# Performance work log

Measured on AMD Instinct MI355X. Metric: run time of the kernel, lower is better.

Reference implementation:

```python
import jax, jax.numpy as jnp
import numpy as np
import math

D_MODEL = 1024
N_HEADS = 16
RANK = 16
SCALE = 16.0
T_LEN = 2048
BSZ = 2


def setup_inputs() -> dict:
    key = jax.random.key(0)
    ks = jax.random.split(key, 12)
    d, r = D_MODEL, RANK
    inp = {
        "query": jax.random.normal(ks[0], (T_LEN, BSZ, d), dtype=jnp.float32),
        "key": jax.random.normal(ks[1], (T_LEN, BSZ, d), dtype=jnp.float32),
        "value": jax.random.normal(ks[2], (T_LEN, BSZ, d), dtype=jnp.float32),
        "need_weights": 0,
        "attn_mask": 0,
        "in_proj_weight": jax.random.normal(ks[3], (3 * d, d), dtype=jnp.float32) * 0.02,
        "in_proj_bias": jax.random.normal(ks[4], (3 * d,), dtype=jnp.float32) * 0.02,
        "out_w": jax.random.normal(ks[5], (d, d), dtype=jnp.float32) * 0.02,
        "out_b": jax.random.normal(ks[6], (d,), dtype=jnp.float32) * 0.02,
        "k_a": jax.random.normal(ks[7], (r, d), dtype=jnp.float32) * 0.02,
        "k_b": jax.random.normal(ks[8], (r, d), dtype=jnp.float32) * 0.02,
        "v_a": jax.random.normal(ks[9], (r, d), dtype=jnp.float32) * 0.02,
        "v_b": jax.random.normal(ks[10], (r, d), dtype=jnp.float32) * 0.02,
    }
    return inp


def reference(query, key, value, need_weights, attn_mask,
              in_proj_weight, in_proj_bias, out_w, out_b,
              k_a, k_b, v_a, v_b):
    # NOTE: original module computes q,k,v all from `query` (self-attention);
    # `key`, `value`, `need_weights`, `attn_mask` are unused in the math.
    T, B, d = query.shape
    H = N_HEADS
    hd = d // H
    qkv = query @ in_proj_weight.T + in_proj_bias  # (T, B, 3d)
    q, k, v = jnp.split(qkv, 3, axis=-1)
    s = SCALE / RANK
    # LoRA low-rank updates on K and V (computed from query)
    k = k + s * ((query @ k_a.T) @ k_b)
    v = v + s * ((query @ v_a.T) @ v_b)
    # split heads: (T, B, H, hd)
    qh = q.reshape(T, B, H, hd)
    kh = k.reshape(T, B, H, hd)
    vh = v.reshape(T, B, H, hd)
    scale = 1.0 / math.sqrt(hd)
    scores = jnp.einsum('tbhd,sbhd->bhts', qh * scale, kh)  # (B, H, T, T)
    attn = jax.nn.softmax(scores, axis=-1)
    out = jnp.einsum('bhts,sbhd->tbhd', attn, vh).reshape(T, B, d)
    out = out @ out_w.T + out_b
    return out
```

## Files before the change

kernel.cpp:

```cpp
#include <hip/hip_runtime.h>
#include <stdint.h>

#define DEVI __device__ __forceinline__

typedef unsigned short u16;
typedef __attribute__((ext_vector_type(4))) float f32x4;
typedef __attribute__((ext_vector_type(16))) float f32x16;
typedef __attribute__((ext_vector_type(8))) short bf16x8;
typedef __attribute__((ext_vector_type(2))) unsigned int u32x2;

constexpr int T_LEN = 2048;
constexpr int BSZ   = 2;
constexpr int DM    = 1024;
constexpr int NH    = 16;
constexpr int HD    = 64;
constexpr int MROWS = T_LEN * BSZ;
constexpr float LORA_S = 16.0f / 16.0f;
constexpr float QSCALE = 0.125f * 1.4426950408889634f;

DEVI u16 f2bf(float x) {
  union { float f; uint32_t u; } v; v.f = x;
  uint32_t r = (v.u + 0x7FFFu + ((v.u >> 16) & 1u)) >> 16;
  return (u16)r;
}

DEVI uint32_t pk2bf(float a, float b) {
  return (uint32_t)f2bf(a) | ((uint32_t)f2bf(b) << 16);
}

DEVI uint32_t e2r(float x) {
  union { float f; uint32_t u; } v;
  v.f = __builtin_amdgcn_exp2f(x);
  return v.u;
}

DEVI void gload_lds16(const void* g, void* l) {
  __builtin_amdgcn_global_load_lds(
      (const __attribute__((address_space(1))) void*)g,
      (__attribute__((address_space(3))) void*)l, 16, 0, 0);
}

DEVI f32x4 mfma16(bf16x8 a, bf16x8 b, f32x4 c) {
  return __builtin_amdgcn_mfma_f32_16x16x32_bf16(a, b, c, 0, 0, 0);
}
DEVI f32x16 mfma32(bf16x8 a, bf16x8 b, f32x16 c) {
  return __builtin_amdgcn_mfma_f32_32x32x16_bf16(a, b, c, 0, 0, 0);
}

DEVI int kvswz(int rc, int l) { return rc * 128 + ((l ^ (rc & 15)) << 3); }

#define WAITBAR(N)                                        \
  do {                                                    \
    asm volatile("s_waitcnt vmcnt(" #N ")" ::: "memory"); \
    __builtin_amdgcn_sched_barrier(0);                    \
    __builtin_amdgcn_s_barrier();                         \
    __builtin_amdgcn_sched_barrier(0);                    \
  } while (0)

#define BARO()                                            \
  do {                                                    \
    __builtin_amdgcn_sched_barrier(0);                    \
    __builtin_amdgcn_s_barrier();                         \
    __builtin_amdgcn_sched_barrier(0);                    \
  } while (0)

__global__ void prep_kernel(const float* __restrict__ query,
                            const float* __restrict__ W,
                            const float* __restrict__ ka, const float* __restrict__ kb,
                            const float* __restrict__ va, const float* __restrict__ vb,
                            const float* __restrict__ ow,
                            u16* __restrict__ Wm, u16* __restrict__ Wo,
                            u16* __restrict__ Aq) {
  const int W3 = 3 * DM * DM;
  const int WO = DM * DM;
  const int AQ = MROWS * DM;
  const int total = W3 + WO + AQ;
  for (int idx = blockIdx.x * blockDim.x + threadIdx.x; idx < total;
       idx += gridDim.x * blockDim.x) {
    if (idx < W3) {
      const int n = idx >> 10, k = idx & 1023;
      float w = W[idx];
      if (n >= 2 * DM) {
        const int n2 = n - 2 * DM;
        float a = 0.f;
#pragma unroll
        for (int r = 0; r < 16; ++r) a += va[r * DM + k] * vb[r * DM + n2];
        w += LORA_S * a;
      } else if (n >= DM) {
        const int n2 = n - DM;
        float a = 0.f;
#pragma unroll
        for (int r = 0; r < 16; ++r) a += ka[r * DM + k] * kb[r * DM + n2];
        w += LORA_S * a;
      }
      Wm[idx] = f2bf(w);
    } else if (idx < W3 + WO) {
      const int i = idx - W3;
      Wo[i] = f2bf(ow[i]);
    } else {
      const int i = idx - W3 - WO;
      Aq[i] = f2bf(query[i]);
    }
  }
}

template <int EPIL>
__global__ __launch_bounds__(256) void gemm_bt(
    const u16* __restrict__ A, const u16* __restrict__ Bt,
    const float* __restrict__ bias, float* __restrict__ Cf,
    u16* __restrict__ Qb, u16* __restrict__ Kb, u16* __restrict__ Vt,
    int M, int N, int K) {
  constexpr int BM = 128, BN = 128, BK = 32;
  __shared__ alignas(16) u16 SM[4][2][4096];
  const int tid = threadIdx.x;
  const int wv = tid >> 6, ln = tid & 63;
  const int l16 = ln & 15, lhi = ln >> 4;
  const int row0 = blockIdx.x * BM, col0 = blockIdx.y * BN;
  const int wr = (wv >> 1) * 64, wc = (wv & 1) * 64;

  f32x4 acc[4][4];
#pragma unroll
  for (int i = 0; i < 4; ++i)
#pragma unroll
    for (int j2 = 0; j2 < 4; ++j2) acc[i][j2] = f32x4{0.f, 0.f, 0.f, 0.f};

  const int lrA = wv * 16 + (ln >> 3);
  const int lrB = lrA + 8;
  const int s_ = ln & 7;
  const int la = s_ ^ (lrA & 7), lb = s_ ^ (lrB & 7);
  const int ra = lrA + 64 * (la >> 2), ca = (la & 3) * 8;
  const int rb = lrB + 64 * (lb >> 2), cb = (lb & 3) * 8;

  const u16* pa0 = A + (size_t)(row0 + ra) * K + ca;
  const u16* pa1 = A + (size_t)(row0 + rb) * K + cb;
  const u16* pb0 = Bt + (size_t)(col0 + ra) * K + ca;
  const u16* pb1 = Bt + (size_t)(col0 + rb) * K + cb;

  auto stagep = [&](int buf) {
    gload_lds16(pa0, &SM[buf][0][(wv * 16) * 64]);
    gload_lds16(pa1, &SM[buf][0][(wv * 16 + 8) * 64]);
    gload_lds16(pb0, &SM[buf][1][(wv * 16) * 64]);
    gload_lds16(pb1, &SM[buf][1][(wv * 16 + 8) * 64]);
    pa0 += BK; pa1 += BK; pb0 += BK; pb1 += BK;
  };

  auto compute = [&](int buf) {
    const u16* Al = SM[buf][0];
    const u16* Bl = SM[buf][1];
    bf16x8 af[4], bfr[4];
#pragma unroll
    for (int m = 0; m < 4; ++m) {
      const int r = wr + m * 16 + l16, lr = r & 63;
      const int sl = (lhi | ((r >> 6) << 2)) ^ (lr & 7);
      af[m] = *(const bf16x8*)&Al[lr * 64 + sl * 8];
    }
#pragma unroll
    for (int n = 0; n < 4; ++n) {
      const int r = wc + n * 16 + l16, lr = r & 63;
      const int sl = (lhi | ((r >> 6) << 2)) ^ (lr & 7);
      bfr[n] = *(const bf16x8*)&Bl[lr * 64 + sl * 8];
    }
#pragma unroll
    for (int m = 0; m < 4; ++m)
#pragma unroll
      for (int n = 0; n < 4; ++n) acc[m][n] = mfma16(af[m], bfr[n], acc[m][n]);
  };

  const int NS = K / BK;
  stagep(0); stagep(1); stagep(2);

  for (int t4 = 0; t4 < NS - 4; t4 += 4) {
    WAITBAR(8); compute(0); stagep(3);
    WAITBAR(8); compute(1); stagep(0);
    WAITBAR(8); compute(2); stagep(1);
    WAITBAR(8); compute(3); stagep(2);
  }
  WAITBAR(8); compute(0); stagep(3);
  WAITBAR(8); compute(1);
  WAITBAR(4); compute(2);
  WAITBAR(0); compute(3);

  if constexpr (EPIL == 0) {
    if (col0 >= 2 * DM) {
      u16* Cl = (u16*)SM;
      __syncthreads();
#pragma unroll
      for (int m = 0; m < 4; ++m)
#pragma unroll
        for (int n = 0; n < 4; ++n) {
          const int lc = wc + n * 16 + l16;
          const float bc = bias[col0 + lc];
#pragma unroll
          for (int r = 0; r < 4; ++r) {
            const int rl = wr + m * 16 + lhi * 4 + r;
            const int tl = rl >> 1, bb = rl & 1;
            Cl[lc * 128 + bb * 64 + (((tl >> 3) ^ (lc & 7)) << 3) + (tl & 7)] =
                f2bf(acc[m][n][r] + bc);
          }
        }
      __syncthreads();
      const int h0 = (col0 - 2 * DM) >> 6;
      const int t0 = row0 >> 1;
#pragma unroll
      for (int i = 0; i < 8; ++i) {
        const int cid = i * 256 + tid;
        const int lc = cid >> 4, bb = (cid >> 3) & 1, tc = cid & 7;
        bf16x8 ch = *(const bf16x8*)&Cl[lc * 128 + bb * 64 + ((tc ^ (lc & 7)) << 3)];
        const int h = h0 + (lc >> 6), dd = lc & 63;
        *(bf16x8*)&Vt[(((size_t)(bb * NH + h)) * HD + dd) * T_LEN + t0 + tc * 8] = ch;
      }
      return;
    }
  }

#pragma unroll
  for (int m = 0; m < 4; ++m) {
#pragma unroll
    for (int n = 0; n < 4; ++n) {
      const int col = col0 + wc + n * 16 + l16;
      const float bc = bias[col];
#pragma unroll
      for (int r = 0; r < 4; ++r) {
        const int row = row0 + wr + m * 16 + lhi * 4 + r;
        const float v = acc[m][n][r] + bc;
        if constexpr (EPIL == 0) {
          const int t = row >> 1, b = row & 1;
          if (col < DM) {
            const int h = col >> 6, dd = col & 63;
            Qb[(((size_t)(b * NH + h)) * T_LEN + t) * HD + dd] = f2bf(v * QSCALE);
          } else {
            const int c2 = col - DM, h = c2 >> 6, dd = c2 & 63;
            Kb[(((size_t)(b * NH + h)) * T_LEN + t) * HD + dd] = f2bf(v);
          }
        } else {
          Cf[(size_t)row * N + col] = v;
        }
      }
    }
  }
}

__global__ __launch_bounds__(256) void attn_kernel(const u16* __restrict__ Qb,
                                                   const u16* __restrict__ Kb,
                                                   const u16* __restrict__ Vt,
                                                   u16* __restrict__ Ob) {
  constexpr int KBLK = 64;
  __shared__ alignas(16) u16 KV[4][2][32 * 128];

  const int tid = threadIdx.x;
  const int wv = tid >> 6, ln = tid & 63;
  const int l32 = ln & 31, hi = ln >> 5;

  const int bid = blockIdx.x;
  const int lb = (bid & 7) * 64 + (bid >> 3);
  const int bh = lb >> 4;
  const int b = bh >> 4, h = bh & 15;
  const int q0 = (lb & 15) * 128 + wv * 32;

  const u16* Qh = Qb + (size_t)bh * T_LEN * HD;
  const u16* Kh = Kb + (size_t)bh * T_LEN * HD;
  const u16* Vh = Vt + (size_t)bh * HD * T_LEN;

  bf16x8 qf[4];
#pragma unroll
  for (int kd = 0; kd < 4; ++kd)
    qf[kd] = *(const bf16x8*)&Qh[(size_t)(q0 + l32) * HD + kd * 16 + hi * 8];

  bf16x8 ones;
#pragma unroll
  for (int i = 0; i < 8; ++i) ones[i] = (short)0x3F80;

  f32x16 ot[2] = {f32x16{}, f32x16{}};
  f32x16 lacc = f32x16{};

  const int g_row = ln >> 4;
  const int g_s   = ln & 15;
  const int j0 = wv * 2, j1 = wv * 2 + 1;
  const int row0r = 4 * j0 + g_row, row1r = 4 * j1 + g_row;
  const int l0 = g_s ^ (row0r & 15), l1 = g_s ^ (row1r & 15);
  const int lr0 = row0r + 32 * (l0 >> 3), lr1 = row1r + 32 * (l1 >> 3);
  const int c80 = (l0 & 7) * 8, c81 = (l1 & 7) * 8;

  const u16* ks0 = Kh + (size_t)lr0 * HD + c80;
  const u16* ks1 = Kh + (size_t)lr1 * HD + c81;
  const u16* vs0 = Vh + (size_t)lr0 * T_LEN + c80;
  const u16* vs1 = Vh + (size_t)lr1 * T_LEN + c81;

  auto stagep = [&](int buf) {
    gload_lds16(ks0, &KV[buf][0][j0 * 512]);
    gload_lds16(ks1, &KV[buf][0][j1 * 512]);
    gload_lds16(vs0, &KV[buf][1][j0 * 512]);
    gload_lds16(vs1, &KV[buf][1][j1 * 512]);
    ks0 += KBLK * HD; ks1 += KBLK * HD; vs0 += KBLK; vs1 += KBLK;
  };

  auto compute = [&](int buf) {
    const u16* Kl = KV[buf][0];
    const u16* Vl = KV[buf][1];
    f32x16 st[2] = {f32x16{}, f32x16{}};
    __builtin_amdgcn_s_setprio(1);
#pragma unroll
    for (int kd = 0; kd < 4; ++kd) {
      bf16x8 k0 = *(const bf16x8*)&Kl[kvswz(l32, kd * 2 + hi)];
      bf16x8 k1 = *(const bf16x8*)&Kl[kvswz(l32, 8 + kd * 2 + hi)];
      st[0] = mfma32(k0, qf[kd], st[0]);
      st[1] = mfma32(k1, qf[kd], st[1]);
    }
    __builtin_amdgcn_s_setprio(0);
    uint32_t c[2][8];
#pragma unroll
    for (int mk = 0; mk < 2; ++mk)
#pragma unroll
      for (int d = 0; d < 8; ++d)
        c[mk][d] = __builtin_amdgcn_perm(e2r(st[mk][2 * d + 1]),
                                         e2r(st[mk][2 * d]), 0x07060302u);
    __builtin_amdgcn_s_setprio(1);
#pragma unroll
    for (int ksl = 0; ksl < 4; ++ksl) {
      const int mk = ksl >> 1, s2 = ksl & 1;
      uint32_t a0 = c[mk][4 * s2 + 0], b0 = c[mk][4 * s2 + 2];
      uint32_t a1 = c[mk][4 * s2 + 1], b1 = c[mk][4 * s2 + 3];
      u32x2 r0 = __builtin_amdgcn_permlane32_swap(a0, b0, false, false);
      u32x2 r1 = __builtin_amdgcn_permlane32_swap(a1, b1, false, false);
      union { bf16x8 v; uint32_t u[4]; } pu;
      pu.u[0] = r0[0]; pu.u[1] = r1[0]; pu.u[2] = r0[1]; pu.u[3] = r1[1];
      bf16x8 vf0 = *(const bf16x8*)&Vl[kvswz(l32, ksl * 2 + hi)];
      bf16x8 vf1 = *(const bf16x8*)&Vl[kvswz(l32, 8 + ksl * 2 + hi)];
      ot[0] = mfma32(vf0, pu.v, ot[0]);
      ot[1] = mfma32(vf1, pu.v, ot[1]);
      lacc = mfma32(ones, pu.v, lacc);
    }
    __builtin_amdgcn_s_setprio(0);
  };

  stagep(0); stagep(1); stagep(2); stagep(3);

  for (int it7 = 0; it7 < 7; ++it7) {
    WAITBAR(8); compute(0); compute(1); BARO(); stagep(0); stagep(1);
    WAITBAR(8); compute(2); compute(3); BARO(); stagep(2); stagep(3);
  }
  WAITBAR(8); compute(0); compute(1);
  WAITBAR(0); compute(2); compute(3);

  const float inv = 1.0f / lacc[0];
  const size_t rowbase = ((size_t)(q0 + l32) * BSZ + b) * DM + h * HD;
#pragma unroll
  for (int dt = 0; dt < 2; ++dt) {
#pragma unroll
    for (int g = 0; g < 4; ++g) {
      const float v0 = ot[dt][4 * g + 0] * inv;
      const float v1 = ot[dt][4 * g + 1] * inv;
      const float v2 = ot[dt][4 * g + 2] * inv;
      const float v3 = ot[dt][4 * g + 3] * inv;
      u32x2 w; w[0] = pk2bf(v0, v1); w[1] = pk2bf(v2, v3);
      const int dim = dt * 32 + 8 * g + 4 * hi;
      *(u32x2*)&Ob[rowbase + dim] = w;
    }
  }
}

extern "C" void kernel_launch(void* const* d_in, const int* in_sizes, int n_in,
                              void* d_out, int out_size, void* d_ws, size_t ws_size,
                              hipStream_t stream) {
  const float* query = (const float*)d_in[0];
  const float* W     = (const float*)d_in[5];
  const float* bias  = (const float*)d_in[6];
  const float* ow    = (const float*)d_in[7];
  const float* ob    = (const float*)d_in[8];
  const float* ka    = (const float*)d_in[9];
  const float* kb    = (const float*)d_in[10];
  const float* va    = (const float*)d_in[11];
  const float* vb    = (const float*)d_in[12];

  char* ws = (char*)d_ws;
  u16* Wm = (u16*)ws; ws += (size_t)3 * DM * DM * 2;
  u16* Wo = (u16*)ws; ws += (size_t)DM * DM * 2;
  u16* Aq = (u16*)ws; ws += (size_t)MROWS * DM * 2;
  u16* Qb = (u16*)ws; ws += (size_t)BSZ * NH * T_LEN * HD * 2;
  u16* Kb = (u16*)ws; ws += (size_t)BSZ * NH * T_LEN * HD * 2;
  u16* Vt = (u16*)ws; ws += (size_t)BSZ * NH * T_LEN * HD * 2;
  u16* Ob = (u16*)ws; ws += (size_t)MROWS * DM * 2;

  prep_kernel<<<2048, 256, 0, stream>>>(query, W, ka, kb, va, vb, ow, Wm, Wo, Aq);

  gemm_bt<0><<<dim3(MROWS / 128, (3 * DM) / 128), 256, 0, stream>>>(
      Aq, Wm, bias, nullptr, Qb, Kb, Vt, MROWS, 3 * DM, DM);

  attn_kernel<<<512, 256, 0, stream>>>(Qb, Kb, Vt, Ob);

  gemm_bt<1><<<dim3(MROWS / 128, DM / 128), 256, 0, stream>>>(
      Ob, Wo, ob, (float*)d_out, nullptr, nullptr, nullptr, MROWS, DM, DM);
}
```

Baseline: 109.7 us.

## Use 256x256-tile, 512-thread GEMM for the fused QKV projection

Adds a dedicated QKV projection kernel with 256x256 output tiles and 8 waves per block in place of the 128x128 templated GEMM, and strips the QKV epilogue from the generic GEMM. Larger tiles double operand reuse from LDS and halve global loads per FLOP, and s_setprio raises the MFMA wave priority. In exchange the grid drops to 16x12=192 blocks, which may underfill the GPU's compute units, and the bigger accumulator footprint raises register pressure.

```diff
diff --git a/kernel.cpp b/kernel.cpp
--- a/kernel.cpp
+++ b/kernel.cpp
@@ -104,6 +104,135 @@
   }
 }
 
+__global__ __launch_bounds__(512) void gemm256_qkv(
+    const u16* __restrict__ A, const u16* __restrict__ Bt,
+    const float* __restrict__ bias,
+    u16* __restrict__ Qb, u16* __restrict__ Kb, u16* __restrict__ Vt) {
+  constexpr int K = DM;
+  constexpr int BK = 32;
+  __shared__ alignas(16) u16 SM[4][2][128 * 64];
+  const int tid = threadIdx.x;
+  const int wv = tid >> 6, ln = tid & 63;
+  const int l16 = ln & 15, lhi = ln >> 4;
+  const int wm = wv >> 2, wn = wv & 3;
+  const int row0 = blockIdx.x * 256, col0 = blockIdx.y * 256;
+
+  f32x4 acc[8][4];
+#pragma unroll
+  for (int m = 0; m < 8; ++m)
+#pragma unroll
+    for (int n = 0; n < 4; ++n) acc[m][n] = f32x4{0.f, 0.f, 0.f, 0.f};
+
+  const int rr0 = wv * 16 + (ln >> 3);
+  const int sl_ = ln & 7;
+  const int v0 = sl_ ^ (rr0 & 7);
+  const int lrow0 = rr0 + 128 * (v0 >> 2);
+  const int c0 = (v0 & 3) * 8;
+
+  const u16* pa = A + (size_t)(row0 + lrow0) * K + c0;
+  const u16* pb = Bt + (size_t)(col0 + lrow0) * K + c0;
+
+  auto stagep = [&](int buf) {
+    gload_lds16(pa, &SM[buf][0][(wv * 16) * 64]);
+    gload_lds16(pa + (size_t)8 * K, &SM[buf][0][(wv * 16 + 8) * 64]);
+    gload_lds16(pb, &SM[buf][1][(wv * 16) * 64]);
+    gload_lds16(pb + (size_t)8 * K, &SM[buf][1][(wv * 16 + 8) * 64]);
+    pa += BK; pb += BK;
+  };
+
+  auto compute = [&](int buf) {
+    const u16* Al = SM[buf][0];
+    const u16* Bl = SM[buf][1];
+    bf16x8 af[8], bfr[4];
+#pragma unroll
+    for (int m = 0; m < 8; ++m) {
+      const int rr = m * 16 + l16;
+      const int sl = (lhi | (wm << 2)) ^ (rr & 7);
+      af[m] = *(const bf16x8*)&Al[rr * 64 + sl * 8];
+    }
+#pragma unroll
+    for (int n = 0; n < 4; ++n) {
+      const int c = wn * 64 + n * 16 + l16;
+      const int rr = c & 127;
+      const int sl = (lhi | ((c >> 7) << 2)) ^ (rr & 7);
+      bfr[n] = *(const bf16x8*)&Bl[rr * 64 + sl * 8];
+    }
+    __builtin_amdgcn_s_setprio(1);
+#pragma unroll
+    for (int m = 0; m < 8; ++m)
+#pragma unroll
+      for (int n = 0; n < 4; ++n) acc[m][n] = mfma16(af[m], bfr[n], acc[m][n]);
+    __builtin_amdgcn_s_setprio(0);
+  };
+
+  constexpr int NS = K / BK;
+  stagep(0); stagep(1); stagep(2);
+
+  for (int t4 = 0; t4 < NS - 4; t4 += 4) {
+    WAITBAR(8); compute(0); stagep(3);
+    WAITBAR(8); compute(1); stagep(0);
+    WAITBAR(8); compute(2); stagep(1);
+    WAITBAR(8); compute(3); stagep(2);
+  }
+  WAITBAR(8); compute(0); stagep(3);
+  WAITBAR(8); compute(1);
+  WAITBAR(4); compute(2);
+  WAITBAR(0); compute(3);
+
+  if (col0 >= 2 * DM) {
+    u16* Cl = (u16*)SM;
+    __syncthreads();
+#pragma unroll
+    for (int m = 0; m < 8; ++m)
+#pragma unroll
+      for (int n = 0; n < 4; ++n) {
+        const int lc = wn * 64 + n * 16 + l16;
+        const float bc = bias[col0 + lc];
+#pragma unroll
+        for (int r = 0; r < 4; ++r) {
+          const int rl = wm * 128 + m * 16 + lhi * 4 + r;
+          const int tl = rl >> 1, bb = rl & 1;
+          Cl[lc * 256 + bb * 128 + (((tl >> 3) ^ (lc & 7)) << 3) + (tl & 7)] =
+              f2bf(acc[m][n][r] + bc);
+        }
+      }
+    __syncthreads();
+    const int h0 = (col0 - 2 * DM) >> 6;
+    const int t0 = row0 >> 1;
+#pragma unroll
+    for (int i = 0; i < 16; ++i) {
+      const int cid = i * 512 + tid;
+      const int lc = cid >> 5, bb = (cid >> 4) & 1, tc = cid & 15;
+      bf16x8 ch = *(const bf16x8*)&Cl[lc * 256 + bb * 128 + ((tc ^ (lc & 7)) << 3)];
+      const int h = h0 + (lc >> 6), dd = lc & 63;
+      *(bf16x8*)&Vt[(((size_t)(bb * NH + h)) * HD + dd) * T_LEN + t0 + tc * 8] = ch;
+    }
+    return;
+  }
+
+#pragma unroll
+  for (int m = 0; m < 8; ++m) {
+#pragma unroll
+    for (int n = 0; n < 4; ++n) {
+      const int col = col0 + wn * 64 + n * 16 + l16;
+      const float bc = bias[col];
+#pragma unroll
+      for (int r = 0; r < 4; ++r) {
+        const int row = row0 + wm * 128 + m * 16 + lhi * 4 + r;
+        const float v = acc[m][n][r] + bc;
+        const int t = row >> 1, b = row & 1;
+        if (col < DM) {
+          const int h = col >> 6, dd = col & 63;
+          Qb[(((size_t)(b * NH + h)) * T_LEN + t) * HD + dd] = f2bf(v * QSCALE);
+        } else {
+          const int c2 = col - DM, h = c2 >> 6, dd = c2 & 63;
+          Kb[(((size_t)(b * NH + h)) * T_LEN + t) * HD + dd] = f2bf(v);
+        }
+      }
+    }
+  }
+}
+
 template <int EPIL>
 __global__ __launch_bounds__(256) void gemm_bt(
     const u16* __restrict__ A, const u16* __restrict__ Bt,
@@ -180,39 +309,6 @@
   WAITBAR(4); compute(2);
   WAITBAR(0); compute(3);
 
-  if constexpr (EPIL == 0) {
-    if (col0 >= 2 * DM) {
-      u16* Cl = (u16*)SM;
-      __syncthreads();
-#pragma unroll
-      for (int m = 0; m < 4; ++m)
-#pragma unroll
-        for (int n = 0; n < 4; ++n) {
-          const int lc = wc + n * 16 + l16;
-          const float bc = bias[col0 + lc];
-#pragma unroll
-          for (int r = 0; r < 4; ++r) {
-            const int rl = wr + m * 16 + lhi * 4 + r;
-            const int tl = rl >> 1, bb = rl & 1;
-            Cl[lc * 128 + bb * 64 + (((tl >> 3) ^ (lc & 7)) << 3) + (tl & 7)] =
-                f2bf(acc[m][n][r] + bc);
-          }
-        }
-      __syncthreads();
-      const int h0 = (col0 - 2 * DM) >> 6;
-      const int t0 = row0 >> 1;
-#pragma unroll
-      for (int i = 0; i < 8; ++i) {
-        const int cid = i * 256 + tid;
-        const int lc = cid >> 4, bb = (cid >> 3) & 1, tc = cid & 7;
-        bf16x8 ch = *(const bf16x8*)&Cl[lc * 128 + bb * 64 + ((tc ^ (lc & 7)) << 3)];
-        const int h = h0 + (lc >> 6), dd = lc & 63;
-        *(bf16x8*)&Vt[(((size_t)(bb * NH + h)) * HD + dd) * T_LEN + t0 + tc * 8] = ch;
-      }
-      return;
-    }
-  }
-
 #pragma unroll
   for (int m = 0; m < 4; ++m) {
 #pragma unroll
@@ -223,18 +319,7 @@
       for (int r = 0; r < 4; ++r) {
         const int row = row0 + wr + m * 16 + lhi * 4 + r;
         const float v = acc[m][n][r] + bc;
-        if constexpr (EPIL == 0) {
-          const int t = row >> 1, b = row & 1;
-          if (col < DM) {
-            const int h = col >> 6, dd = col & 63;
-            Qb[(((size_t)(b * NH + h)) * T_LEN + t) * HD + dd] = f2bf(v * QSCALE);
-          } else {
-            const int c2 = col - DM, h = c2 >> 6, dd = c2 & 63;
-            Kb[(((size_t)(b * NH + h)) * T_LEN + t) * HD + dd] = f2bf(v);
-          }
-        } else {
-          Cf[(size_t)row * N + col] = v;
-        }
+        Cf[(size_t)row * N + col] = v;
       }
     }
   }
@@ -383,8 +468,8 @@
 
   prep_kernel<<<2048, 256, 0, stream>>>(query, W, ka, kb, va, vb, ow, Wm, Wo, Aq);
 
-  gemm_bt<0><<<dim3(MROWS / 128, (3 * DM) / 128), 256, 0, stream>>>(
-      Aq, Wm, bias, nullptr, Qb, Kb, Vt, MROWS, 3 * DM, DM);
+  gemm256_qkv<<<dim3(MROWS / 256, (3 * DM) / 256), 512, 0, stream>>>(
+      Aq, Wm, bias, Qb, Kb, Vt);
 
   attn_kernel<<<512, 256, 0, stream>>>(Qb, Kb, Vt, Ob);
 
```

Result: no change. 110.9 us (+1.1%).
